# Kernel tuning notes

Hardware: AMD Instinct MI355X
Metric: run time of the kernel (lower is better)

The kernel has to match this reference:

```python
import jax, jax.numpy as jnp
import numpy as np

V, P, C, M, P_ORIG, T = 81920, 131072, 512, 1024, 163840, 262144


def setup_inputs() -> dict:
    key = jax.random.key(0)
    ks = jax.random.split(key, 6)
    adapter_feat = jax.random.normal(ks[0], (V, C), dtype=jnp.float32)
    ce = jax.random.normal(ks[1], (M, C), dtype=jnp.float32)
    # caption embeddings arrive pre-normalized in the original pipeline
    caption_embed = ce / jnp.clip(jnp.linalg.norm(ce, axis=-1, keepdims=True), 1e-12)
    logit_scale = jnp.full((1,), np.log(1.0 / 0.07), dtype=jnp.float32)  # learnable param init
    v2p_map = jax.random.randint(ks[2], (P,), 0, V, dtype=jnp.int32)
    origin_idx = jax.random.randint(ks[3], (P,), 0, P_ORIG, dtype=jnp.int32)
    caption_to_point_mapping = jax.random.randint(ks[4], (T,), 0, P_ORIG, dtype=jnp.int32)
    caption_seg_idx = jnp.sort(jax.random.randint(ks[5], (T,), 0, M, dtype=jnp.int32))
    return {
        "adapter_feat": adapter_feat,
        "caption_embed": caption_embed,
        "logit_scale": logit_scale,
        "v2p_map": v2p_map,
        "origin_idx": origin_idx,
        "caption_to_point_mapping": caption_to_point_mapping,
        "caption_seg_idx": caption_seg_idx,
        "n_origin_points": P_ORIG,
    }


def reference(adapter_feat, caption_embed, logit_scale, v2p_map, origin_idx,
              caption_to_point_mapping, caption_seg_idx, n_origin_points):
    n_pts = v2p_map.shape[0]
    n_captions = caption_embed.shape[0]

    # gather voxel features to points, L2-normalize (feat_norm=True)
    feats = adapter_feat[v2p_map]                                       # [P, C]
    feats = feats / jnp.clip(jnp.linalg.norm(feats, axis=-1, keepdims=True), 1e-12)

    # per-point log-softmax caption scores
    logits = (feats @ caption_embed.T) * jnp.exp(logit_scale[0])        # [P, M]
    scores = jax.nn.log_softmax(logits, axis=-1)                        # [P, M]

    # origin-point -> current-point mapping; -1 where origin point was dropped
    ptom = jnp.full((n_origin_points,), -1, dtype=jnp.int32)
    ptom = ptom.at[origin_idx].set(jnp.arange(n_pts, dtype=jnp.int32))

    gidx = ptom[caption_to_point_mapping]                               # [T]
    invalid = (gidx < 0).astype(scores.dtype)                           # [T]
    # torch negative advanced indexing wraps; replicate faithfully
    safe = jnp.where(gidx < 0, gidx + n_pts, gidx)
    gathered = scores[safe]                                             # [T, M]

    # scatter-sum scores and counts per caption segment
    pooled = jax.ops.segment_sum(gathered, caption_seg_idx, num_segments=n_captions)
    cnt = jax.ops.segment_sum(jnp.ones_like(invalid), caption_seg_idx, num_segments=n_captions)
    ninv = jax.ops.segment_sum(invalid, caption_seg_idx, num_segments=n_captions)
    real_n_points = cnt - ninv                                          # [N]

    denom = jnp.where(real_n_points > 0,
                      1.0 / jnp.where(real_n_points > 0, real_n_points, 1.0), 0.0)
    pooled = pooled * denom[:, None]                                    # [N, M]
    if_has_pts = real_n_points > 0
    return pooled, real_n_points, if_has_pts
```

## Files before the change

### kernel.cpp

```cpp
#include <hip/hip_runtime.h>

#define P_PTS 131072
#define CDIM  512
#define MCAP  1024
#define TLEN  262144
#define PORIG 163840

typedef unsigned short u16;
typedef unsigned char  u8;
typedef __attribute__((ext_vector_type(8))) short short8;
typedef __attribute__((ext_vector_type(4))) float f32x4;
typedef __attribute__((ext_vector_type(8))) int int8v;
typedef __attribute__((ext_vector_type(4))) int int4v;

__device__ __forceinline__ u16 f2bf(float f) {
    unsigned u = __float_as_uint(f);
    unsigned r = (u + 0x7FFFu + ((u >> 16) & 1u)) >> 16;
    return (u16)r;
}
__device__ __forceinline__ float d_e4m3(unsigned x) {
    float f = __uint_as_float((x & 0x7Fu) << 20) * 0x1p120f;
    return __uint_as_float(__float_as_uint(f) | ((x & 0x80u) << 24));
}
__device__ __forceinline__ void ld16(const void* g, void* l) {
    __builtin_amdgcn_global_load_lds(
        (const __attribute__((address_space(1))) void*)g,
        (__attribute__((address_space(3))) void*)l, 16, 0, 0);
}


__global__ __launch_bounds__(256) void gather_prep(
    const float* __restrict__ adapter, const int* __restrict__ v2p,
    const float* __restrict__ cap, const int* __restrict__ oidx,
    u8* __restrict__ feats8, u16* __restrict__ capb, u8* __restrict__ Bswz,
    int* __restrict__ ptom, float* __restrict__ lse_sum) {
    __shared__ __align__(16) u8 sm[4 * 544];
    int b = blockIdx.x, tid = threadIdx.x;
    if (b < 32768) {
        int w = tid >> 6, lane = tid & 63;
        int p = b * 4 + w;
        int vrow = v2p[p];
        const float4* src = (const float4*)(adapter + (size_t)vrow * CDIM);
        float4 x0 = src[lane * 2];
        float4 x1 = src[lane * 2 + 1];
        float ss = x0.x*x0.x + x0.y*x0.y + x0.z*x0.z + x0.w*x0.w
                 + x1.x*x1.x + x1.y*x1.y + x1.z*x1.z + x1.w*x1.w;
        #pragma unroll
        for (int off = 32; off >= 1; off >>= 1) ss += __shfl_xor(ss, off, 64);
        float inv = 1.0f / fmaxf(sqrtf(ss), 1e-12f);
        int lo = __builtin_amdgcn_cvt_pk_fp8_f32(x0.x*inv, x0.y*inv, 0, false);
        lo = __builtin_amdgcn_cvt_pk_fp8_f32(x0.z*inv, x0.w*inv, lo, true);
        int hi = __builtin_amdgcn_cvt_pk_fp8_f32(x1.x*inv, x1.y*inv, 0, false);
        hi = __builtin_amdgcn_cvt_pk_fp8_f32(x1.z*inv, x1.w*inv, hi, true);
        uint2 wv; wv.x = (unsigned)lo; wv.y = (unsigned)hi;
        *(uint2*)(sm + w * 544 + lane * 8) = wv;
        __syncthreads();
        int chunk = tid >> 4, inner = tid & 15;
        int kk = chunk >> 2, q = chunk & 3, rr = inner >> 2;
        uint2 v = *(const uint2*)(sm + rr * 544 + kk * 128 + q * 32 + (inner & 3) * 8);
        *(uint2*)(feats8 + (size_t)(b >> 2) * 8192 + kk * 2048 + q * 512
                         + (b & 3) * 128 + inner * 8) = v;
    } else if (b < 33280) {
        int t = (b - 32768) * 256 + tid;
        int i = t * 4;
        float4 v = *(const float4*)(cap + i);
        u16* o = capb + i;
        o[0] = f2bf(v.x); o[1] = f2bf(v.y); o[2] = f2bf(v.z); o[3] = f2bf(v.w);
        atomicMax(&ptom[oidx[t]], t);
    } else if (b < 33792) {
        int j = (b - 33280) * 256 + tid;
        lse_sum[j] = 0.0f;
    } else {
        int g2 = (b - 33792) * 256 + tid;
        int c    = g2 & 1;
        int lane = (g2 >> 1) & 63;
        int j    = (g2 >> 7) & 3;
        int kk   = (g2 >> 9) & 3;
        int wn   = (g2 >> 11) & 1;
        int c0   = g2 >> 12;
        int col  = c0 * 128 + wn * 64 + j * 16 + (lane & 15);
        int kb   = kk * 128 + (lane >> 4) * 32 + c * 16;
        const float* s = cap + (size_t)col * CDIM + kb;
        unsigned w4[4];
        #pragma unroll
        for (int u = 0; u < 4; ++u) {
            int p = __builtin_amdgcn_cvt_pk_fp8_f32(s[u*4+0], s[u*4+1], 0, false);
            p = __builtin_amdgcn_cvt_pk_fp8_f32(s[u*4+2], s[u*4+3], p, true);
            w4[u] = (unsigned)p;
        }
        *(uint4*)(Bswz + (size_t)g2 * 16) = *(uint4*)w4;
    }
}

__global__ __launch_bounds__(256, 2) void lse_gemm(
    const u8* __restrict__ feats8, const u8* __restrict__ Bswz,
    const float* __restrict__ lsc, float* __restrict__ lse_sum,
    const int* __restrict__ ctpm, const int* __restrict__ ptom,
    unsigned* __restrict__ rows) {
    if (blockIdx.x >= 1024) {
        int t = (blockIdx.x - 1024) * 256 + threadIdx.x;
        int g = ptom[ctpm[t]];
        rows[t] = (g < 0) ? ((unsigned)(g + P_PTS) | 0x80000000u) : (unsigned)g;
        return;
    }
    __shared__ __align__(16) u8 As[65536];
    const int tid  = threadIdx.x;
    const int wave = tid >> 6;
    const int lane = tid & 63;
    const int bid  = blockIdx.x;
    const int row0 = bid * 128;
    const int wm   = (wave >> 1) * 64;
    const int wn1  = (wave & 1);
    const float sf = __expf(lsc[0]);

    {
        const u8* src = feats8 + (size_t)(bid * 8 + wave * 2) * 8192 + lane * 16;
        u8* dst = As + wave * 2 * 8192;
        #pragma unroll
        for (int cr = 0; cr < 2; ++cr)
            #pragma unroll
            for (int kk = 0; kk < 4; ++kk) {
                ld16(src + cr * 8192 + kk * 2048,        dst + cr * 8192 + kk * 2048);
                ld16(src + cr * 8192 + kk * 2048 + 1024, dst + cr * 8192 + kk * 2048 + 1024);
            }
    }
    asm volatile("s_waitcnt vmcnt(0)" ::: "memory");
    __builtin_amdgcn_sched_barrier(0);
    __builtin_amdgcn_s_barrier();
    __builtin_amdgcn_sched_barrier(0);

    const int m = lane & 15;
    const int q = lane >> 4;
    const u8* rA = As + (size_t)(wave >> 1) * 32768 + lane * 32;

    float ssum[4][4];
    #pragma unroll
    for (int i = 0; i < 4; ++i)
        #pragma unroll
        for (int r = 0; r < 4; ++r) ssum[i][r] = 0.f;

    #pragma unroll 1
    for (int c0 = 0; c0 < 8; ++c0) {
        const u8* bw = Bswz + (size_t)(c0 * 2 + wn1) * 32768 + lane * 32;
        f32x4 acc[4][4] = {};
        #pragma unroll
        for (int kk = 0; kk < 4; ++kk) {
            int8v bv[4];
            #pragma unroll
            for (int j = 0; j < 4; ++j) {
                int4v lo = *(const int4v*)(bw + (kk * 4 + j) * 2048);
                int4v hi = *(const int4v*)(bw + (kk * 4 + j) * 2048 + 16);
                bv[j][0]=lo[0]; bv[j][1]=lo[1]; bv[j][2]=lo[2]; bv[j][3]=lo[3];
                bv[j][4]=hi[0]; bv[j][5]=hi[1]; bv[j][6]=hi[2]; bv[j][7]=hi[3];
            }
            int8v af[4];
            #pragma unroll
            for (int i = 0; i < 4; ++i) {
                const u8* a = rA + i * 8192 + kk * 2048;
                int4v lo = *(const int4v*)(a);
                int4v hi = *(const int4v*)(a + 16);
                af[i][0]=lo[0]; af[i][1]=lo[1]; af[i][2]=lo[2]; af[i][3]=lo[3];
                af[i][4]=hi[0]; af[i][5]=hi[1]; af[i][6]=hi[2]; af[i][7]=hi[3];
            }
            #pragma unroll
            for (int i = 0; i < 4; ++i)
                #pragma unroll
                for (int j = 0; j < 4; ++j)
                    acc[i][j] = __builtin_amdgcn_mfma_scale_f32_16x16x128_f8f6f4(
                        af[i], bv[j], acc[i][j], 0, 0, 0, 127, 0, 127);
        }
        #pragma unroll
        for (int i = 0; i < 4; ++i) {
            float s4[4] = {0.f, 0.f, 0.f, 0.f};
            #pragma unroll
            for (int j = 0; j < 4; ++j)
                #pragma unroll
                for (int r = 0; r < 4; ++r)
                    s4[r] += __expf(acc[i][j][r] * sf - sf);
            #pragma unroll
            for (int off = 8; off >= 1; off >>= 1)
                #pragma unroll
                for (int r = 0; r < 4; ++r)
                    s4[r] += __shfl_xor(s4[r], off, 64);
            #pragma unroll
            for (int r = 0; r < 4; ++r) ssum[i][r] += s4[r];
        }
    }
    if (m == 0) {
        #pragma unroll
        for (int i = 0; i < 4; ++i) {
            int rbase = row0 + wm + i * 16 + q * 4;
            #pragma unroll
            for (int r = 0; r < 4; ++r)
                lse_sum[rbase + r] = ssum[i][r];
        }
    }
}

__device__ __forceinline__ int lower_bound(const int* __restrict__ a, int n, int key) {
    int lo = 0, hi = n;
    while (lo < hi) { int mid = (lo + hi) >> 1; if (a[mid] < key) lo = mid + 1; else hi = mid; }
    return lo;
}

__global__ __launch_bounds__(1024) void seg_reduce(
    const u8* __restrict__ feats8, const float* __restrict__ lse_sum,
    const unsigned* __restrict__ rows, const int* __restrict__ seg,
    const float* __restrict__ lsc,
    u16* __restrict__ Fb, float* __restrict__ Lout, float* __restrict__ realn) {
    int s = blockIdx.x;
    int tid = threadIdx.x, wave = tid >> 6, lane = tid & 63;
    int start = lower_bound(seg, TLEN, s);
    int end   = lower_bound(seg, TLEN, s + 1);
    const int loff = (lane >> 4) * 2048 + ((lane >> 2) & 3) * 512 + (lane & 3) * 8;
    const int chb  = (lane >> 4) * 128  + ((lane >> 2) & 3) * 32  + (lane & 3) * 8;
    float a[8] = {0,0,0,0,0,0,0,0};
    float Lacc = 0.f; int inv = 0;
    int r = start + wave;
    for (; r + 16 < end; r += 32) {
        unsigned p0 = rows[r], p1 = rows[r + 16];
        int r0 = (int)(p0 & 0x7FFFFFFFu), r1 = (int)(p1 & 0x7FFFFFFFu);
        uint2 v0 = *(const uint2*)(feats8 + (size_t)(r0 >> 4) * 8192 + (r0 & 15) * 32 + loff);
        uint2 v1 = *(const uint2*)(feats8 + (size_t)(r1 >> 4) * 8192 + (r1 & 15) * 32 + loff);
        if (lane == 0) {
            inv += (int)(p0 >> 31) + (int)(p1 >> 31);
            Lacc += __logf(lse_sum[r0]) + __logf(lse_sum[r1]);
        }
        a[0] += d_e4m3(v0.x);       a[1] += d_e4m3(v0.x >> 8);
        a[2] += d_e4m3(v0.x >> 16); a[3] += d_e4m3(v0.x >> 24);
        a[4] += d_e4m3(v0.y);       a[5] += d_e4m3(v0.y >> 8);
        a[6] += d_e4m3(v0.y >> 16); a[7] += d_e4m3(v0.y >> 24);
        a[0] += d_e4m3(v1.x);       a[1] += d_e4m3(v1.x >> 8);
        a[2] += d_e4m3(v1.x >> 16); a[3] += d_e4m3(v1.x >> 24);
        a[4] += d_e4m3(v1.y);       a[5] += d_e4m3(v1.y >> 8);
        a[6] += d_e4m3(v1.y >> 16); a[7] += d_e4m3(v1.y >> 24);
    }
    if (r < end) {
        unsigned p0 = rows[r];
        int r0 = (int)(p0 & 0x7FFFFFFFu);
        uint2 v0 = *(const uint2*)(feats8 + (size_t)(r0 >> 4) * 8192 + (r0 & 15) * 32 + loff);
        if (lane == 0) { inv += (int)(p0 >> 31); Lacc += __logf(lse_sum[r0]); }
        a[0] += d_e4m3(v0.x);       a[1] += d_e4m3(v0.x >> 8);
        a[2] += d_e4m3(v0.x >> 16); a[3] += d_e4m3(v0.x >> 24);
        a[4] += d_e4m3(v0.y);       a[5] += d_e4m3(v0.y >> 8);
        a[6] += d_e4m3(v0.y >> 16); a[7] += d_e4m3(v0.y >> 24);
    }
    __shared__ float pF[16][512];
    __shared__ float pL[16];
    __shared__ int   pI[16];
    #pragma unroll
    for (int u = 0; u < 8; ++u) pF[wave][chb + u] = a[u];
    if (lane == 0) { pL[wave] = Lacc; pI[wave] = inv; }
    __syncthreads();
    if (tid < 512) {
        float f = 0.f;
        #pragma unroll
        for (int w = 0; w < 16; ++w) f += pF[w][tid];
        Fb[(size_t)s * CDIM + tid] = f2bf(f);
    }
    if (tid == 0) {
        float cnt = (float)(end - start);
        float Ls = 0.f; int ninv = 0;
        #pragma unroll
        for (int w = 0; w < 16; ++w) { Ls += pL[w]; ninv += pI[w]; }
        realn[s] = cnt - (float)ninv;
        Lout[s] = Ls + __expf(lsc[0]) * cnt;
    }
}

__global__ __launch_bounds__(256) void pooled_gemm(
    const u16* __restrict__ Fb, const u16* __restrict__ capb,
    const float* __restrict__ Lout, const float* __restrict__ realn,
    const float* __restrict__ lsc, float* __restrict__ out) {
    const int tid  = threadIdx.x;
    const int wave = tid >> 6;
    const int lane = tid & 63;
    const int col0 = blockIdx.x * 64;
    const int row0 = blockIdx.y * 64;
    const int wm = (wave >> 1) * 32;
    const int wn = (wave & 1) * 32;
    const float sf = __expf(lsc[0]);
    f32x4 acc[2][2] = {};
    const int mrow = lane & 15;
    const int quad = lane >> 4;
    const u16* gA = Fb   + (size_t)(row0 + wm + mrow) * CDIM + quad * 8;
    const u16* gB = capb + (size_t)(col0 + wn + mrow) * CDIM + quad * 8;
    #pragma unroll
    for (int k0 = 0; k0 < CDIM; k0 += 32) {
        short8 af[2], bfr[2];
        #pragma unroll
        for (int i = 0; i < 2; ++i)
            af[i]  = *(const short8*)(gA + (size_t)(i * 16) * CDIM + k0);
        #pragma unroll
        for (int j = 0; j < 2; ++j)
            bfr[j] = *(const short8*)(gB + (size_t)(j * 16) * CDIM + k0);
        #pragma unroll
        for (int i = 0; i < 2; ++i)
            #pragma unroll
            for (int j = 0; j < 2; ++j)
                acc[i][j] = __builtin_amdgcn_mfma_f32_16x16x32_bf16(
                    af[i], bfr[j], acc[i][j], 0, 0, 0);
    }
    #pragma unroll
    for (int i = 0; i < 2; ++i) {
        #pragma unroll
        for (int r = 0; r < 4; ++r) {
            int s = row0 + wm + i * 16 + quad * 4 + r;
            float rn = realn[s];
            float dn = rn > 0.f ? 1.0f / rn : 0.0f;
            float L = Lout[s];
            #pragma unroll
            for (int j = 0; j < 2; ++j) {
                int mc = col0 + wn + j * 16 + mrow;
                out[(size_t)s * MCAP + mc] = (sf * acc[i][j][r] - L) * dn;
            }
        }
    }
    if (col0 == 0 && tid < 64) {
        int s = row0 + tid;
        float rv = realn[s];
        out[MCAP * MCAP + s] = rv;
        out[MCAP * MCAP + MCAP + s] = (rv > 0.f) ? 1.0f : 0.0f;
    }
}

extern "C" void kernel_launch(void* const* d_in, const int* in_sizes, int n_in,
                              void* d_out, int out_size, void* d_ws, size_t ws_size,
                              hipStream_t stream) {
    const float* adapter = (const float*)d_in[0];
    const float* cap     = (const float*)d_in[1];
    const float* lsc     = (const float*)d_in[2];
    const int*   v2p     = (const int*)d_in[3];
    const int*   oidx    = (const int*)d_in[4];
    const int*   ctpm    = (const int*)d_in[5];
    const int*   seg     = (const int*)d_in[6];
    float* out = (float*)d_out;

    char* ws = (char*)d_ws;
    u8*       feats8  = (u8*)(ws);
    u16*      capb    = (u16*)(ws + 67108864);
    u8*       Bswz    = (u8*)(ws + 68157440);
    float*    lse_sum = (float*)(ws + 68681728);
    int*      ptom    = (int*)(ws + 69206016);
    unsigned* rows    = (unsigned*)(ws + 69861376);
    u16*      Fb      = (u16*)(ws + 70909952);
    float*    Lout    = (float*)(ws + 71958528);
    float*    realn   = (float*)(ws + 71962624);

    hipMemsetAsync(ptom, 0xFF, (size_t)PORIG * 4, stream);

    gather_prep<<<33920, 256, 0, stream>>>(adapter, v2p, cap, oidx,
                                           feats8, capb, Bswz, ptom, lse_sum);
    lse_gemm<<<1024 + TLEN / 256, 256, 0, stream>>>(feats8, Bswz, lsc, lse_sum,
                                                    ctpm, ptom, rows);
    seg_reduce<<<MCAP, 1024, 0, stream>>>(feats8, lse_sum, rows, seg, lsc, Fb, Lout, realn);
    pooled_gemm<<<dim3(MCAP / 64, MCAP / 64), 256, 0, stream>>>(Fb, capb, Lout, realn, lsc, out);
}
```

Baseline: 424.4 us.

## Double-buffer B fragments in registers and defer the row-sum shuffle reduction

In the fp8 MFMA logsumexp kernel, the B-operand LDS reads for the next k-step are now issued before the current step's MFMAs, into a two-slot register buffer. This lets LDS latency overlap with matrix math, and `s_setprio` raises wave priority around the MFMA block. Per-row exp partial sums are kept per lane across all column chunks, and the cross-lane shuffle reduction runs once at the end instead of once per chunk. Results are written with `atomicAdd` so that waves covering different column halves of the same rows combine correctly. This relies on `lse_sum` being zeroed beforehand and adds register pressure.

```diff
diff --git a/kernel.cpp b/kernel.cpp
--- a/kernel.cpp
+++ b/kernel.cpp
@@ -12,6 +12,8 @@
 typedef __attribute__((ext_vector_type(4))) float f32x4;
 typedef __attribute__((ext_vector_type(8))) int int8v;
 typedef __attribute__((ext_vector_type(4))) int int4v;
+
+union V32 { int8v v8; int4v v4[2]; };
 
 __device__ __forceinline__ u16 f2bf(float f) {
     unsigned u = __float_as_uint(f);
@@ -132,69 +134,69 @@
     const int m = lane & 15;
     const int q = lane >> 4;
     const u8* rA = As + (size_t)(wave >> 1) * 32768 + lane * 32;
-
-    float ssum[4][4];
+    const u8* bb = Bswz + (size_t)wn1 * 32768 + lane * 32;
+
+    V32 bbuf[2][4];
+    #pragma unroll
+    for (int j = 0; j < 4; ++j) {
+        bbuf[0][j].v4[0] = *(const int4v*)(bb + j * 2048);
+        bbuf[0][j].v4[1] = *(const int4v*)(bb + j * 2048 + 16);
+    }
+
+    float psum[4][4];
     #pragma unroll
     for (int i = 0; i < 4; ++i)
         #pragma unroll
-        for (int r = 0; r < 4; ++r) ssum[i][r] = 0.f;
+        for (int r = 0; r < 4; ++r) psum[i][r] = 0.f;
 
     #pragma unroll 1
     for (int c0 = 0; c0 < 8; ++c0) {
-        const u8* bw = Bswz + (size_t)(c0 * 2 + wn1) * 32768 + lane * 32;
         f32x4 acc[4][4] = {};
         #pragma unroll
         for (int kk = 0; kk < 4; ++kk) {
-            int8v bv[4];
-            #pragma unroll
-            for (int j = 0; j < 4; ++j) {
-                int4v lo = *(const int4v*)(bw + (kk * 4 + j) * 2048);
-                int4v hi = *(const int4v*)(bw + (kk * 4 + j) * 2048 + 16);
-                bv[j][0]=lo[0]; bv[j][1]=lo[1]; bv[j][2]=lo[2]; bv[j][3]=lo[3];
-                bv[j][4]=hi[0]; bv[j][5]=hi[1]; bv[j][6]=hi[2]; bv[j][7]=hi[3];
+            if (c0 < 7 || kk < 3) {
+                const u8* p = bb + (size_t)c0 * 65536
+                                 + (kk < 3 ? (kk + 1) * 8192 : 65536);
+                #pragma unroll
+                for (int j = 0; j < 4; ++j) {
+                    bbuf[(kk + 1) & 1][j].v4[0] = *(const int4v*)(p + j * 2048);
+                    bbuf[(kk + 1) & 1][j].v4[1] = *(const int4v*)(p + j * 2048 + 16);
+                }
             }
-            int8v af[4];
+            V32 af[4];
             #pragma unroll
             for (int i = 0; i < 4; ++i) {
-                const u8* a = rA + i * 8192 + kk * 2048;
-                int4v lo = *(const int4v*)(a);
-                int4v hi = *(const int4v*)(a + 16);
-                af[i][0]=lo[0]; af[i][1]=lo[1]; af[i][2]=lo[2]; af[i][3]=lo[3];
-                af[i][4]=hi[0]; af[i][5]=hi[1]; af[i][6]=hi[2]; af[i][7]=hi[3];
+                af[i].v4[0] = *(const int4v*)(rA + i * 8192 + kk * 2048);
+                af[i].v4[1] = *(const int4v*)(rA + i * 8192 + kk * 2048 + 16);
             }
+            __builtin_amdgcn_s_setprio(1);
             #pragma unroll
             for (int i = 0; i < 4; ++i)
                 #pragma unroll
                 for (int j = 0; j < 4; ++j)
                     acc[i][j] = __builtin_amdgcn_mfma_scale_f32_16x16x128_f8f6f4(
-                        af[i], bv[j], acc[i][j], 0, 0, 0, 127, 0, 127);
-        }
-        #pragma unroll
-        for (int i = 0; i < 4; ++i) {
-            float s4[4] = {0.f, 0.f, 0.f, 0.f};
+                        af[i].v8, bbuf[kk & 1][j].v8, acc[i][j],
+                        0, 0, 0, 127, 0, 127);
+            __builtin_amdgcn_s_setprio(0);
+        }
+        #pragma unroll
+        for (int i = 0; i < 4; ++i)
             #pragma unroll
             for (int j = 0; j < 4; ++j)
                 #pragma unroll
                 for (int r = 0; r < 4; ++r)
-                    s4[r] += __expf(acc[i][j][r] * sf - sf);
-            #pragma unroll
-            for (int off = 8; off >= 1; off >>= 1)
-                #pragma unroll
-                for (int r = 0; r < 4; ++r)
-                    s4[r] += __shfl_xor(s4[r], off, 64);
-            #pragma unroll
-            for (int r = 0; r < 4; ++r) ssum[i][r] += s4[r];
-        }
-    }
-    if (m == 0) {
-        #pragma unroll
-        for (int i = 0; i < 4; ++i) {
-            int rbase = row0 + wm + i * 16 + q * 4;
-            #pragma unroll
-            for (int r = 0; r < 4; ++r)
-                lse_sum[rbase + r] = ssum[i][r];
-        }
-    }
+                    psum[i][r] += __expf(acc[i][j][r] * sf - sf);
+    }
+    #pragma unroll
+    for (int i = 0; i < 4; ++i)
+        #pragma unroll
+        for (int r = 0; r < 4; ++r) {
+            float v = psum[i][r];
+            #pragma unroll
+            for (int off = 8; off >= 1; off >>= 1) v += __shfl_xor(v, off, 64);
+            if (m == 0)
+                atomicAdd(&lse_sum[row0 + wm + i * 16 + q * 4 + r], v);
+        }
 }
 
 __device__ __forceinline__ int lower_bound(const int* __restrict__ a, int n, int key) {
```

After: 512.0 us. 20.7% more time.
